# Performance work log

Hardware: AMD Instinct MI355X
Metric: run time of the kernel (lower is better)

## Reference

```python
import jax, jax.numpy as jnp
import numpy as np

B, N, HN, HE, H = 8, 128, 256, 128, 8
DH = HN // H
P = N * (N - 1) // 2


def _ln(x, g, b, eps=1e-5):
    m = jnp.mean(x, axis=-1, keepdims=True)
    v = jnp.mean((x - m) ** 2, axis=-1, keepdims=True)
    return (x - m) * jax.lax.rsqrt(v + eps) * g + b


def setup_inputs() -> dict:
    key = jax.random.key(0)
    ks = jax.random.split(key, 16)
    i1, i2 = np.triu_indices(N, k=1)  # all unordered pairs, P = N(N-1)/2
    s = lambda fan: 1.0 / np.sqrt(fan)
    return {
        "node_feat": jax.random.normal(ks[0], (B, N, HN), jnp.float32),
        "edge_feat": jax.random.normal(ks[1], (B, P, HE), jnp.float32),
        "x_idx1": jnp.asarray(i1, jnp.int32),
        "x_idx2": jnp.asarray(i2, jnp.int32),
        "mask_valid": jax.random.bernoulli(ks[2], 0.9, (B, P)).astype(jnp.float32),
        "Wqkv": jax.random.normal(ks[3], (HN, 3 * HN), jnp.float32) * s(HN),
        "bqkv": jnp.zeros((3 * HN,), jnp.float32),
        "Wev": jax.random.normal(ks[4], (HE, HN), jnp.float32) * s(HE),
        "bev": jnp.zeros((HN,), jnp.float32),
        "Wea": jax.random.normal(ks[5], (HE, H), jnp.float32) * s(HE),
        "bea": jnp.zeros((H,), jnp.float32),
        "Wo": jax.random.normal(ks[6], (2 * HN, HN), jnp.float32) * s(2 * HN),
        "bo": jnp.zeros((HN,), jnp.float32),
        "Wsk": jax.random.normal(ks[7], (HN, 2 * HN), jnp.float32) * s(HN),
        "bsk": jnp.zeros((2 * HN,), jnp.float32),
        "gn": jnp.ones((HN,), jnp.float32),
        "bn": jnp.zeros((HN,), jnp.float32),
        "ge": jnp.ones((HE,), jnp.float32),
        "be": jnp.zeros((HE,), jnp.float32),
    }


def reference(node_feat, edge_feat, x_idx1, x_idx2, mask_valid,
              Wqkv, bqkv, Wev, bev, Wea, bea, Wo, bo, Wsk, bsk,
              gn, bn, ge, be):
    n_in = _ln(node_feat, gn, bn)                      # [B,N,HN]
    e_in = _ln(edge_feat, ge, be)                      # [B,P,HE]
    q, k, v = jnp.split(n_in @ Wqkv + bqkv, 3, axis=-1)
    to_h = lambda t: t.reshape(B, -1, H, DH).transpose(0, 2, 1, 3)
    q, k, v = to_h(q), to_h(k), to_h(v)                # [B,H,N,DH]
    e_val = to_h(e_in @ Wev + bev)                     # [B,H,P,DH]
    e_adj = (e_in @ Wea + bea).transpose(0, 2, 1)      # [B,H,P]

    scale = DH ** -0.5
    logits = jnp.einsum('bhqd,bhkd->bhqk', q, k) * scale  # [B,H,N,N]
    # per-pair logits; torch stacks [qk, edge_adj] then sums -> just add
    l_node1 = logits[:, :, x_idx1, x_idx2] + e_adj     # node i1 attends to i2
    l_node2 = logits[:, :, x_idx2, x_idx1] + e_adj     # node i2 attends to i1
    v_node1 = e_val + v[:, :, x_idx2]                  # value node i1 receives
    v_node2 = e_val + v[:, :, x_idx1]

    # group the 2P directed edges by destination node (= torch cat+sort+reshape)
    cat_idx = jnp.concatenate([x_idx1, x_idx2])        # [2P]
    order = jnp.argsort(cat_idx)                       # stable sort
    gl = jnp.concatenate([l_node1, l_node2], axis=2)[:, :, order].reshape(B, H, N, N - 1)
    gv = jnp.concatenate([v_node1, v_node2], axis=2)[:, :, order].reshape(B, H, N, N - 1, DH)
    gm = jnp.concatenate([mask_valid, mask_valid], axis=1)[:, order].reshape(B, N, N - 1)[:, None]  # [B,1,N,N-1]

    gl = jnp.where(gm == 0.0, -9e15, gl)
    probs = jax.nn.softmax(gl, axis=3)
    probs = probs * jnp.any(gm != 0.0, axis=3, keepdims=True).astype(probs.dtype)
    attn = jnp.einsum('bhnk,bhnkd->bhnd', probs, gv)   # [B,H,N,DH]
    attn = attn.transpose(0, 2, 1, 3).reshape(B, N, HN)

    comb = jax.nn.gelu(jnp.concatenate([n_in, attn], axis=-1) @ Wo + bo, approximate=False)
    val, gate = jnp.split(comb @ Wsk + bsk, 2, axis=-1)
    g = jax.nn.sigmoid(gate)
    return node_feat * (1.0 - g) + val * g
```

## Files before the change

kernel.cpp:

```cpp
#include <hip/hip_runtime.h>
#include <hip/hip_bf16.h>
#include <math.h>

#define BB 8
#define NN 128
#define HN 256
#define HE 128
#define NH 8
#define DH 32
#define PP 8128
#define BP (BB*PP)

typedef __hip_bfloat16 bf16;
typedef __hip_bfloat162 bf162;
typedef __attribute__((ext_vector_type(8))) short bf16x8;
typedef __attribute__((ext_vector_type(4))) float f32x4;

__device__ __forceinline__ float bf2f(bf16 x){ return __bfloat162float(x); }
__device__ __forceinline__ float bfraw2f(short u){
  return __uint_as_float(((unsigned)(unsigned short)u) << 16);
}

__device__ __forceinline__ float wave_sum(float v){
  #pragma unroll
  for (int off=32; off>=1; off>>=1) v += __shfl_xor(v, off, 64);
  return v;
}
__device__ __forceinline__ float g16_sum(float v){
  #pragma unroll
  for (int off=8; off>=1; off>>=1) v += __shfl_xor(v, off, 16);
  return v;
}

__device__ __forceinline__ int pair_idx(int a, int c){
  int i = a < c ? a : c;
  int j = a < c ? c : a;
  return ((i*(255 - i))>>1) + (j - i - 1);
}

#define C_NODE 0LL
#define C_MASK 262144LL
#define C_WQKV 327168LL
#define C_BQKV 523776LL
#define C_WEV  524544LL
#define C_BEV  557312LL
#define C_WEA  557568LL
#define C_BEA  558592LL
#define C_WO   558600LL
#define C_BO   689672LL
#define C_WSK  689928LL
#define C_BSK  821000LL
#define C_GN   821512LL
#define C_BN   821768LL
#define C_GE   822024LL
#define C_BE   822152LL
#define IOFF   822400LL
#define TOT8   102785
#define CONVBLKS 402
#define I_NIN  0LL
#define I_Q    262144LL
#define I_K    524288LL
#define I_V    786432LL
#define I_ATTN 1048576LL
#define I_COMB 1310720LL
#define I_EA2  1572864LL
#define I_XG   2093056LL
#define I_WT   14577664LL
#define I_WOB  14594048LL
#define I_WSKB 14659584LL
#define I_FLG  14725120LL

struct SrcPtrs { const void* p[16]; };

__global__ __launch_bounds__(256) void k_convert(SrcPtrs sp, float* __restrict__ dst,
                                                 int* __restrict__ flags,
                                                 const unsigned short* __restrict__ nodeRaw,
                                                 const void* __restrict__ rawWev,
                                                 bf16* __restrict__ Wt,
                                                 const void* __restrict__ rawWo,
                                                 const void* __restrict__ rawWsk,
                                                 bf16* __restrict__ WoB,
                                                 bf16* __restrict__ WskB)
{
  __shared__ int sbad;
  if (threadIdx.x == 0) sbad = 0;
  __syncthreads();
  {
    int bad = 0;
    for (int i = threadIdx.x; i < 1024; i += 256){
      unsigned e = (nodeRaw[i] >> 7) & 0xFFu;
      if (e >= 194u) bad = 1;
    }
    if (bad) sbad = 1;
  }
  __syncthreads();
  const int f32 = sbad;
  if (blockIdx.x == 0 && threadIdx.x == 0) flags[0] = f32;

  if (blockIdx.x >= CONVBLKS + 128){
    int o = (blockIdx.x - (CONVBLKS + 128))*256 + threadIdx.x;
    const void* src = (o < 16384) ? rawWo : rawWsk;
    bf16* dw = (o < 16384) ? WoB : WskB;
    int lo = (o < 16384) ? o : o - 16384;
    if (f32){
      const float4* s4 = (const float4*)src;
      float4 a0 = s4[2*lo], a1 = s4[2*lo+1];
      union { float4 f; bf16 h[8]; } cv;
      cv.h[0]=__float2bfloat16(a0.x); cv.h[1]=__float2bfloat16(a0.y);
      cv.h[2]=__float2bfloat16(a0.z); cv.h[3]=__float2bfloat16(a0.w);
      cv.h[4]=__float2bfloat16(a1.x); cv.h[5]=__float2bfloat16(a1.y);
      cv.h[6]=__float2bfloat16(a1.z); cv.h[7]=__float2bfloat16(a1.w);
      *reinterpret_cast<float4*>(dw + lo*8) = cv.f;
    } else {
      *reinterpret_cast<float4*>(dw + lo*8) = ((const float4*)src)[lo];
    }
    return;
  }

  if (blockIdx.x >= CONVBLKS){
    int idx = (blockIdx.x - CONVBLKS)*256 + threadIdx.x;
    float v = f32 ? ((const float*)rawWev)[idx]
                  : bfraw2f(((const short*)rawWev)[idx]);
    Wt[(idx & 255)*128 + (idx >> 8)] = __float2bfloat16(v);
    return;
  }

  int o = blockIdx.x*256 + threadIdx.x;
  if (o >= TOT8) return;
  const int cum[17] = {0,32768,40896,65472,65568,69664,69696,69824,69825,
                       86209,86241,102625,102689,102721,102753,102769,102785};
  int s = 0;
  #pragma unroll
  for (int i = 1; i <= 15; i++) if (o >= cum[i]) s = i;
  const int li = o - cum[s];
  float4 r0, r1;
  if (f32){
    const float4* src = (const float4*)sp.p[s];
    r0 = src[2*li]; r1 = src[2*li+1];
  } else {
    union { float4 f; unsigned short u[8]; } cv;
    cv.f = ((const float4*)sp.p[s])[li];
    r0.x = __uint_as_float((unsigned)cv.u[0] << 16);
    r0.y = __uint_as_float((unsigned)cv.u[1] << 16);
    r0.z = __uint_as_float((unsigned)cv.u[2] << 16);
    r0.w = __uint_as_float((unsigned)cv.u[3] << 16);
    r1.x = __uint_as_float((unsigned)cv.u[4] << 16);
    r1.y = __uint_as_float((unsigned)cv.u[5] << 16);
    r1.z = __uint_as_float((unsigned)cv.u[6] << 16);
    r1.w = __uint_as_float((unsigned)cv.u[7] << 16);
  }
  float4* d = (float4*)(dst + (long long)cum[s]*8);
  d[2*li]   = r0;
  d[2*li+1] = r1;
}

__global__ __launch_bounds__(256) void k1_node_ln_qkv(
    const float* __restrict__ cnode, const float* __restrict__ cWqkv,
    const float* __restrict__ cbqkv, const float* __restrict__ cgn, const float* __restrict__ cbn,
    float* __restrict__ nin_ws, float* __restrict__ q_ws, float* __restrict__ k_ws,
    float* __restrict__ v_ws)
{
  __shared__ float xln[4][HN];
  const int t = threadIdx.x, wv = t>>6, lane = t&63;
  const int cb = blockIdx.x % 3;
  const int g0 = (blockIdx.x / 3) * 4;
  {
    int g = g0 + wv;
    float x[4];
    #pragma unroll
    for (int i=0;i<4;i++) x[i] = cnode[g*HN + lane + 64*i];
    float s = x[0]+x[1]+x[2]+x[3];
    s = wave_sum(s);
    float m = s * (1.0f/HN);
    float q = 0.f;
    #pragma unroll
    for (int i=0;i<4;i++){ float d = x[i]-m; q += d*d; }
    q = wave_sum(q);
    float rstd = rsqrtf(fmaxf(q*(1.0f/HN), 0.f) + 1e-5f);
    #pragma unroll
    for (int i=0;i<4;i++){
      int c = lane + 64*i;
      float y = (x[i]-m)*rstd*cgn[c] + cbn[c];
      xln[wv][c] = y;
      if (cb == 0) nin_ws[g*HN + c] = y;
    }
  }
  __syncthreads();
  const int col = cb*256 + t;
  float acc[4];
  {
    float bb = cbqkv[col];
    #pragma unroll
    for (int r=0;r<4;r++) acc[r] = bb;
  }
  for (int k=0;k<HN;k+=4){
    float4 xv[4];
    #pragma unroll
    for (int r=0;r<4;r++) xv[r] = *reinterpret_cast<const float4*>(&xln[r][k]);
    #pragma unroll
    for (int kk=0;kk<4;kk++){
      float w = cWqkv[(k+kk)*768 + col];
      #pragma unroll
      for (int r=0;r<4;r++) acc[r] = fmaf((&xv[r].x)[kk], w, acc[r]);
    }
  }
  if (cb == 2){
    #pragma unroll
    for (int r=0;r<4;r++) v_ws[(long)(g0+r)*HN + t] = acc[r];
  } else {
    float* dstp = (cb == 0) ? q_ws : k_ws;
    const int h = t>>5, d = t&31;
    #pragma unroll
    for (int r=0;r<4;r++){
      int g = g0 + r;
      int b = g>>7, n = g&127;
      dstp[((b*NH + h)*NN + n)*DH + d] = acc[r];
    }
  }
}

__global__ __launch_bounds__(256) void k2a_edge_ln(
    const void* __restrict__ edge_raw, const float* __restrict__ cWea,
    const float* __restrict__ cbea, const float* __restrict__ cge,
    const float* __restrict__ cbe, const float* __restrict__ cmask,
    bf16* __restrict__ xg, float* __restrict__ ea2, const int* __restrict__ flags)
{
  __shared__ float xlnS[16][136];
  __shared__ float part[128];
  const int t = threadIdx.x;
  const int R0 = blockIdx.x*16;
  const int b = R0 / PP;
  const int p0 = R0 - b*PP;
  const int f32 = flags[0];
  {
    int r = t>>4, sub = t&15;
    long base = (long)(R0 + r)*HE + sub*8;
    float x[8];
    if (f32){
      const float* cef = (const float*)edge_raw + base;
      float4 a0 = *reinterpret_cast<const float4*>(cef);
      float4 a1 = *reinterpret_cast<const float4*>(cef + 4);
      x[0]=a0.x; x[1]=a0.y; x[2]=a0.z; x[3]=a0.w;
      x[4]=a1.x; x[5]=a1.y; x[6]=a1.z; x[7]=a1.w;
    } else {
      union { float4 f; short u[8]; } cv;
      cv.f = *reinterpret_cast<const float4*>((const bf16*)edge_raw + base);
      #pragma unroll
      for (int i=0;i<8;i++) x[i] = bfraw2f(cv.u[i]);
    }
    float s = 0.f;
    #pragma unroll
    for (int i=0;i<8;i++) s += x[i];
    s = g16_sum(s);
    float m = s*(1.0f/HE);
    float q = 0.f;
    #pragma unroll
    for (int i=0;i<8;i++){ float dd = x[i]-m; q += dd*dd; }
    q = g16_sum(q);
    float rstd = rsqrtf(fmaxf(q*(1.0f/HE), 0.f) + 1e-5f);
    #pragma unroll
    for (int i=0;i<8;i++){
      int c = sub*8 + i;
      xlnS[r][c] = (x[i]-m)*rstd*cge[c] + cbe[c];
    }
  }
  __syncthreads();
  {
    int r = t>>4, c0 = (t&15)*8;
    union { float4 f; bf16 h[8]; } o;
    #pragma unroll
    for (int i=0;i<8;i++) o.h[i] = __float2bfloat16(xlnS[r][c0+i]);
    *reinterpret_cast<float4*>(xg + (long)(R0 + r)*HE + c0) = o.f;
  }
  {
    const int c = t & 7, r = (t>>3) & 15, half = t>>7;
    const int pid = r*8 + c;
    float s = half ? 0.0f : cbea[c];
    const int k0 = half*64;
    #pragma unroll 8
    for (int k=k0; k<k0+64; k++) s = fmaf(xlnS[r][k], cWea[k*NH + c], s);
    if (half){ part[pid] = s; }
    __syncthreads();
    if (!half){
      s += part[pid];
      int p = p0 + r;
      float mk = cmask[b*PP + p];
      ea2[((long)b*PP + p)*8 + c] = (mk != 0.0f) ? s : -9e15f;
    }
  }
}

__global__ __launch_bounds__(256) void k3_attn(
    const float* __restrict__ q_ws,
    const float* __restrict__ k_ws,
    const float* __restrict__ v_ws,
    const bf16* __restrict__ xg,
    const float* __restrict__ ea2,
    const bf16* __restrict__ Wt,
    const float* __restrict__ cbev,
    float* __restrict__ attn)
{
  __shared__ __align__(16) float qS[8][32];
  __shared__ __align__(16) int   prS[128];
  __shared__ __align__(16) float eaS[128][8];
  __shared__ __align__(16) float pS[8][128];
  __shared__ __align__(16) float sS[8][128];
  __shared__ __align__(16) bf16  xgS[128][128];
  __shared__ float anyS[8];
  const int t = threadIdx.x;
  const int bid = blockIdx.x;
  const int swz = (bid & 7)*128 + (bid >> 3);
  const int n = swz & 127, b = swz >> 7;
  const int h = t >> 5, ln = t & 31;

  qS[h][ln] = q_ws[(((long)b*NH + h)*NN + n)*DH + ln];
  if (t < 128){
    int m = t;
    prS[m] = pair_idx(n, (m == n) ? (m ^ 1) : m);
  }
  __syncthreads();

  const bf16* xgb = xg + (long)b*PP*HE;
  {
    int m = t >> 1, c0 = (t & 1)*4;
    float4 ev = *reinterpret_cast<const float4*>(ea2 + ((long)b*PP + prS[m])*8 + c0);
    *reinterpret_cast<float4*>(&eaS[m][c0]) = ev;
  }
  #pragma unroll
  for (int it=0; it<8; ++it){
    int idx = it*256 + t;
    int row = idx >> 4, seg = idx & 15;
    int pr = prS[row];
    *reinterpret_cast<float4*>(&xgS[row][seg*8]) =
        *reinterpret_cast<const float4*>(xgb + (long)pr*HE + seg*8);
  }
  __syncthreads();

  const float scale = 0.17677669529663687f;
  float4 qv[8];
  #pragma unroll
  for (int d4=0; d4<8; d4++) qv[d4] = *reinterpret_cast<const float4*>(&qS[h][d4*4]);
  const float* kb = k_ws + ((long)b*NH + h)*NN*DH;
  float l[4];
  float mx = -INFINITY;
  int valid = 0;
  #pragma unroll
  for (int j=0;j<4;j++){
    int m = ln + 32*j;
    const float* kr = kb + m*DH;
    float dot = 0.f;
    #pragma unroll
    for (int d4=0; d4<8; d4++){
      float4 kv = *reinterpret_cast<const float4*>(kr + d4*4);
      dot = fmaf((&qv[d4].x)[0], kv.x, dot);
      dot = fmaf((&qv[d4].x)[1], kv.y, dot);
      dot = fmaf((&qv[d4].x)[2], kv.z, dot);
      dot = fmaf((&qv[d4].x)[3], kv.w, dot);
    }
    float eav = eaS[m][h];
    bool self = (m == n);
    l[j] = self ? -INFINITY : fmaf(dot, scale, eav);
    if (!self && eav > -8.9e15f) valid = 1;
    mx = fmaxf(mx, l[j]);
  }
  #pragma unroll
  for (int off=16; off>=1; off>>=1) mx = fmaxf(mx, __shfl_xor(mx, off, 32));
  float e[4], s = 0.f;
  #pragma unroll
  for (int j=0;j<4;j++){ e[j] = __expf(l[j]-mx); s += e[j]; }
  float av = valid ? 1.f : 0.f;
  #pragma unroll
  for (int off=16; off>=1; off>>=1){
    s  += __shfl_xor(s,  off, 32);
    av += __shfl_xor(av, off, 32);
  }
  float inv = (av > 0.f) ? (1.0f/s) : 0.f;
  #pragma unroll
  for (int j=0;j<4;j++) pS[h][ln+32*j] = e[j]*inv;
  if (ln == 0) anyS[h] = (av > 0.f) ? 1.f : 0.f;
  __syncthreads();

  const float* vb = v_ws + (long)b*NN*HN + h*DH + ln;
  float S0=0.f,S1=0.f,S2=0.f,S3=0.f,T=0.f;
  #pragma unroll 2
  for (int m0=0; m0<128; m0+=4){
    float4 p4 = *reinterpret_cast<const float4*>(&pS[h][m0]);
    #pragma unroll
    for (int i=0;i<4;i++){
      float pm = (&p4.x)[i];
      short4 xv = *reinterpret_cast<const short4*>(&xgS[m0+i][ln*4]);
      S0 = fmaf(pm, bfraw2f(xv.x), S0);
      S1 = fmaf(pm, bfraw2f(xv.y), S1);
      S2 = fmaf(pm, bfraw2f(xv.z), S2);
      S3 = fmaf(pm, bfraw2f(xv.w), S3);
      T  = fmaf(pm, vb[(m0+i)*HN], T);
    }
  }
  {
    float4 sv; sv.x=S0; sv.y=S1; sv.z=S2; sv.w=S3;
    *reinterpret_cast<float4*>(&sS[h][ln*4]) = sv;
  }
  __syncthreads();

  float acc = T + anyS[h]*cbev[h*DH + ln];
  const bf16* wr = Wt + (h*DH + ln)*HE;
  #pragma unroll 4
  for (int k0=0;k0<128;k0+=8){
    float4 sa = *reinterpret_cast<const float4*>(&sS[h][k0]);
    float4 sb = *reinterpret_cast<const float4*>(&sS[h][k0+4]);
    bf16x8 wv = *reinterpret_cast<const bf16x8*>(wr + k0);
    acc = fmaf(sa.x, bfraw2f(wv[0]), acc);
    acc = fmaf(sa.y, bfraw2f(wv[1]), acc);
    acc = fmaf(sa.z, bfraw2f(wv[2]), acc);
    acc = fmaf(sa.w, bfraw2f(wv[3]), acc);
    acc = fmaf(sb.x, bfraw2f(wv[4]), acc);
    acc = fmaf(sb.y, bfraw2f(wv[5]), acc);
    acc = fmaf(sb.z, bfraw2f(wv[6]), acc);
    acc = fmaf(sb.w, bfraw2f(wv[7]), acc);
  }
  attn[((long)b*NN + n)*HN + h*DH + ln] = acc;
}

__global__ __launch_bounds__(256) void k4_wo_gelu(
    const float* __restrict__ nin_ws, const float* __restrict__ attn,
    const bf16* __restrict__ WoB, const float* __restrict__ cbo,
    float* __restrict__ comb)
{
  __shared__ float xc[4][512];
  __shared__ float ps[3][4][64];
  const int t = threadIdx.x;
  const int g0 = (blockIdx.x >> 2) * 4;
  const int cq = blockIdx.x & 3;
  {
    int r = t>>6, c0 = (t&63)*8;
    const float* src = (c0 < 256) ? (nin_ws + (long)(g0+r)*HN + c0)
                                  : (attn + (long)(g0+r)*HN + (c0-256));
    float4 a0 = *reinterpret_cast<const float4*>(src);
    float4 a1 = *reinterpret_cast<const float4*>(src+4);
    *reinterpret_cast<float4*>(&xc[r][c0]) = a0;
    *reinterpret_cast<float4*>(&xc[r][c0+4]) = a1;
  }
  __syncthreads();
  const int cidx = t & 63, ks = t >> 6;
  const int col = cq*64 + cidx;
  float acc[4] = {0.f,0.f,0.f,0.f};
  const int k0 = ks*128;
  #pragma unroll 4
  for (int k=k0; k<k0+128; k++){
    float w = bf2f(WoB[k*HN + col]);
    #pragma unroll
    for (int r=0;r<4;r++) acc[r] = fmaf(xc[r][k], w, acc[r]);
  }
  if (ks){
    #pragma unroll
    for (int r=0;r<4;r++) ps[ks-1][r][cidx] = acc[r];
  }
  __syncthreads();
  if (!ks){
    float bb = cbo[col];
    #pragma unroll
    for (int r=0;r<4;r++){
      float x = acc[r] + bb + ps[0][r][cidx] + ps[1][r][cidx] + ps[2][r][cidx];
      comb[(long)(g0+r)*HN + col] = 0.5f*x*(1.0f + erff(x*0.7071067811865475f));
    }
  }
}

__global__ __launch_bounds__(256) void k5_sk_gate(
    const float* __restrict__ comb, const float* __restrict__ cnode,
    const bf16* __restrict__ WskB, const float* __restrict__ cbsk,
    void* __restrict__ out, const int* __restrict__ flags)
{
  __shared__ float xc[4][HN];
  __shared__ float psv[3][4][64];
  __shared__ float psg[3][4][64];
  const int t = threadIdx.x;
  const int g0 = (blockIdx.x >> 2) * 4;
  const int cq = blockIdx.x & 3;
  {
    int r = t>>6, c0 = (t&63)*4;
    *reinterpret_cast<float4*>(&xc[r][c0]) =
        *reinterpret_cast<const float4*>(comb + (long)(g0+r)*HN + c0);
  }
  __syncthreads();
  const int cidx = t & 63, ks = t >> 6;
  const int col = cq*64 + cidx;
  float av[4] = {0.f,0.f,0.f,0.f}, ag[4] = {0.f,0.f,0.f,0.f};
  const int k0 = ks*64;
  #pragma unroll 4
  for (int k=k0; k<k0+64; k++){
    float wv = bf2f(WskB[k*512 + col]);
    float wg = bf2f(WskB[k*512 + col + 256]);
    #pragma unroll
    for (int r=0;r<4;r++){
      float xr = xc[r][k];
      av[r] = fmaf(xr, wv, av[r]);
      ag[r] = fmaf(xr, wg, ag[r]);
    }
  }
  if (ks){
    #pragma unroll
    for (int r=0;r<4;r++){ psv[ks-1][r][cidx] = av[r]; psg[ks-1][r][cidx] = ag[r]; }
  }
  __syncthreads();
  if (!ks){
    const int f32 = flags[0];
    float bv = cbsk[col], bg = cbsk[col+256];
    #pragma unroll
    for (int r=0;r<4;r++){
      float v = av[r] + bv + psv[0][r][cidx] + psv[1][r][cidx] + psv[2][r][cidx];
      float g = ag[r] + bg + psg[0][r][cidx] + psg[1][r][cidx] + psg[2][r][cidx];
      float gg = 1.0f/(1.0f + __expf(-g));
      float nf = cnode[(long)(g0+r)*HN + col];
      float res = nf*(1.0f - gg) + v*gg;
      if (f32) ((float*)out)[(long)(g0+r)*HN + col] = res;
      else ((bf16*)out)[(long)(g0+r)*HN + col] = __float2bfloat16(res);
    }
  }
}

extern "C" void kernel_launch(void* const* d_in, const int* in_sizes, int n_inputs,
                              void* d_out, int out_size, void* d_ws, size_t ws_size,
                              hipStream_t stream)
{
  float* ws = (float*)d_ws;
  float* c_node = ws + C_NODE;
  float* c_mask = ws + C_MASK;
  float* c_Wqkv = ws + C_WQKV;
  float* c_bqkv = ws + C_BQKV;
  float* c_bev  = ws + C_BEV;
  float* c_Wea  = ws + C_WEA;
  float* c_bea  = ws + C_BEA;
  float* c_bo   = ws + C_BO;
  float* c_bsk  = ws + C_BSK;
  float* c_gn   = ws + C_GN;
  float* c_bn   = ws + C_BN;
  float* c_ge   = ws + C_GE;
  float* c_be   = ws + C_BE;
  float* base   = ws + IOFF;
  float* nin_ws  = base + I_NIN;
  float* q_ws    = base + I_Q;
  float* k_ws    = base + I_K;
  float* v_ws    = base + I_V;
  float* attn_ws = base + I_ATTN;
  float* comb_ws = base + I_COMB;
  float* ea2_ws  = base + I_EA2;
  bf16*  xg_ws   = (bf16*)(base + I_XG);
  bf16*  wt_ws   = (bf16*)(base + I_WT);
  bf16*  wob_ws  = (bf16*)(base + I_WOB);
  bf16*  wskb_ws = (bf16*)(base + I_WSKB);
  int*   flags   = (int*)(base + I_FLG);

  SrcPtrs sp;
  sp.p[0]  = d_in[0];
  sp.p[1]  = d_in[4];
  sp.p[2]  = d_in[5];
  sp.p[3]  = d_in[6];
  sp.p[4]  = d_in[7];
  sp.p[5]  = d_in[8];
  sp.p[6]  = d_in[9];
  sp.p[7]  = d_in[10];
  sp.p[8]  = d_in[11];
  sp.p[9]  = d_in[12];
  sp.p[10] = d_in[13];
  sp.p[11] = d_in[14];
  sp.p[12] = d_in[15];
  sp.p[13] = d_in[16];
  sp.p[14] = d_in[17];
  sp.p[15] = d_in[18];

  k_convert<<<CONVBLKS + 256, 256, 0, stream>>>(sp, ws, flags,
                                                (const unsigned short*)d_in[0],
                                                d_in[7], wt_ws,
                                                d_in[11], d_in[13],
                                                wob_ws, wskb_ws);
  k1_node_ln_qkv<<<768, 256, 0, stream>>>(c_node, c_Wqkv, c_bqkv, c_gn, c_bn,
                                          nin_ws, q_ws, k_ws, v_ws);
  k2a_edge_ln<<<BP/16, 256, 0, stream>>>(d_in[1], c_Wea, c_bea, c_ge, c_be, c_mask,
                                         xg_ws, ea2_ws, flags);
  k3_attn<<<BB*NN, 256, 0, stream>>>(q_ws, k_ws, v_ws, xg_ws, ea2_ws, wt_ws, c_bev,
                                     attn_ws);
  k4_wo_gelu<<<1024, 256, 0, stream>>>(nin_ws, attn_ws, wob_ws, c_bo, comb_ws);
  k5_sk_gate<<<1024, 256, 0, stream>>>(comb_ws, c_node, wskb_ws, c_bsk, d_out, flags);
}
```

Before: 198.0 us.

## Prefetch gathered edge rows into registers and overlap with logit computation

The attention kernel now loads q and the edge logit bias straight from global memory into registers and removes the shared staging arrays for them, along with two block barriers. The gathered edge-feature rows are loaded into registers before the QK/softmax phase and written to shared memory only afterward, so global gather latency overlaps with the logit math. Softmax probabilities are broadcast with wave shuffles instead of shared memory, and an occupancy hint of 4 blocks is added. The cost is higher register pressure from holding 8 float4 prefetches plus q, which the launch-bounds hint may force into spills.

Measured after the change: 198.0 us. About the same (+0.0%).

```diff
diff --git a/kernel.cpp b/kernel.cpp
--- a/kernel.cpp
+++ b/kernel.cpp
@@ -290,7 +290,7 @@
   }
 }
 
-__global__ __launch_bounds__(256) void k3_attn(
+__global__ __launch_bounds__(256, 4) void k3_attn(
     const float* __restrict__ q_ws,
     const float* __restrict__ k_ws,
     const float* __restrict__ v_ws,
@@ -300,46 +300,38 @@
     const float* __restrict__ cbev,
     float* __restrict__ attn)
 {
-  __shared__ __align__(16) float qS[8][32];
-  __shared__ __align__(16) int   prS[128];
-  __shared__ __align__(16) float eaS[128][8];
-  __shared__ __align__(16) float pS[8][128];
+  __shared__ __align__(16) bf16  xgS[128][128];
   __shared__ __align__(16) float sS[8][128];
-  __shared__ __align__(16) bf16  xgS[128][128];
-  __shared__ float anyS[8];
   const int t = threadIdx.x;
   const int bid = blockIdx.x;
   const int swz = (bid & 7)*128 + (bid >> 3);
   const int n = swz & 127, b = swz >> 7;
   const int h = t >> 5, ln = t & 31;
 
-  qS[h][ln] = q_ws[(((long)b*NH + h)*NN + n)*DH + ln];
-  if (t < 128){
-    int m = t;
-    prS[m] = pair_idx(n, (m == n) ? (m ^ 1) : m);
-  }
-  __syncthreads();
-
+  float4 qv[8];
+  const float* qb = q_ws + (((long)b*NH + h)*NN + n)*DH;
+  #pragma unroll
+  for (int d4=0; d4<8; d4++) qv[d4] = *reinterpret_cast<const float4*>(qb + d4*4);
+  float eav[4];
+  const float* eab = ea2 + (long)b*PP*8;
+  #pragma unroll
+  for (int j=0;j<4;j++){
+    int m = ln + 32*j;
+    int ms = (m == n) ? (m ^ 1) : m;
+    eav[j] = eab[(long)pair_idx(n, ms)*8 + h];
+  }
   const bf16* xgb = xg + (long)b*PP*HE;
-  {
-    int m = t >> 1, c0 = (t & 1)*4;
-    float4 ev = *reinterpret_cast<const float4*>(ea2 + ((long)b*PP + prS[m])*8 + c0);
-    *reinterpret_cast<float4*>(&eaS[m][c0]) = ev;
-  }
+  const int rowb = t >> 4, seg = t & 15;
+  float4 xr[8];
   #pragma unroll
   for (int it=0; it<8; ++it){
-    int idx = it*256 + t;
-    int row = idx >> 4, seg = idx & 15;
-    int pr = prS[row];
-    *reinterpret_cast<float4*>(&xgS[row][seg*8]) =
-        *reinterpret_cast<const float4*>(xgb + (long)pr*HE + seg*8);
-  }
-  __syncthreads();
+    int row = it*16 + rowb;
+    int ms = (row == n) ? (row ^ 1) : row;
+    int pr = pair_idx(n, ms);
+    xr[it] = *reinterpret_cast<const float4*>(xgb + (long)pr*HE + seg*8);
+  }
 
   const float scale = 0.17677669529663687f;
-  float4 qv[8];
-  #pragma unroll
-  for (int d4=0; d4<8; d4++) qv[d4] = *reinterpret_cast<const float4*>(&qS[h][d4*4]);
   const float* kb = k_ws + ((long)b*NH + h)*NN*DH;
   float l[4];
   float mx = -INFINITY;
@@ -352,15 +344,14 @@
     #pragma unroll
     for (int d4=0; d4<8; d4++){
       float4 kv = *reinterpret_cast<const float4*>(kr + d4*4);
-      dot = fmaf((&qv[d4].x)[0], kv.x, dot);
-      dot = fmaf((&qv[d4].x)[1], kv.y, dot);
-      dot = fmaf((&qv[d4].x)[2], kv.z, dot);
-      dot = fmaf((&qv[d4].x)[3], kv.w, dot);
-    }
-    float eav = eaS[m][h];
+      dot = fmaf(qv[d4].x, kv.x, dot);
+      dot = fmaf(qv[d4].y, kv.y, dot);
+      dot = fmaf(qv[d4].z, kv.z, dot);
+      dot = fmaf(qv[d4].w, kv.w, dot);
+    }
     bool self = (m == n);
-    l[j] = self ? -INFINITY : fmaf(dot, scale, eav);
-    if (!self && eav > -8.9e15f) valid = 1;
+    l[j] = self ? -INFINITY : fmaf(dot, scale, eav[j]);
+    if (!self && eav[j] > -8.9e15f) valid = 1;
     mx = fmaxf(mx, l[j]);
   }
   #pragma unroll
@@ -375,25 +366,33 @@
     av += __shfl_xor(av, off, 32);
   }
   float inv = (av > 0.f) ? (1.0f/s) : 0.f;
-  #pragma unroll
-  for (int j=0;j<4;j++) pS[h][ln+32*j] = e[j]*inv;
-  if (ln == 0) anyS[h] = (av > 0.f) ? 1.f : 0.f;
+  float pj0 = e[0]*inv, pj1 = e[1]*inv, pj2 = e[2]*inv, pj3 = e[3]*inv;
+
+  #pragma unroll
+  for (int it=0; it<8; ++it){
+    int row = it*16 + rowb;
+    *reinterpret_cast<float4*>(&xgS[row][seg*8]) = xr[it];
+  }
   __syncthreads();
 
   const float* vb = v_ws + (long)b*NN*HN + h*DH + ln;
   float S0=0.f,S1=0.f,S2=0.f,S3=0.f,T=0.f;
-  #pragma unroll 2
-  for (int m0=0; m0<128; m0+=4){
-    float4 p4 = *reinterpret_cast<const float4*>(&pS[h][m0]);
-    #pragma unroll
-    for (int i=0;i<4;i++){
-      float pm = (&p4.x)[i];
-      short4 xv = *reinterpret_cast<const short4*>(&xgS[m0+i][ln*4]);
-      S0 = fmaf(pm, bfraw2f(xv.x), S0);
-      S1 = fmaf(pm, bfraw2f(xv.y), S1);
-      S2 = fmaf(pm, bfraw2f(xv.z), S2);
-      S3 = fmaf(pm, bfraw2f(xv.w), S3);
-      T  = fmaf(pm, vb[(m0+i)*HN], T);
+  #pragma unroll
+  for (int j=0;j<4;j++){
+    float pcur = (j==0) ? pj0 : (j==1) ? pj1 : (j==2) ? pj2 : pj3;
+    #pragma unroll 2
+    for (int mm=0; mm<32; mm+=4){
+      #pragma unroll
+      for (int i=0;i<4;i++){
+        int m = j*32 + mm + i;
+        float pm = __shfl(pcur, mm + i, 32);
+        short4 xv = *reinterpret_cast<const short4*>(&xgS[m][ln*4]);
+        S0 = fmaf(pm, bfraw2f(xv.x), S0);
+        S1 = fmaf(pm, bfraw2f(xv.y), S1);
+        S2 = fmaf(pm, bfraw2f(xv.z), S2);
+        S3 = fmaf(pm, bfraw2f(xv.w), S3);
+        T  = fmaf(pm, vb[m*HN], T);
+      }
     }
   }
   {
@@ -402,7 +401,7 @@
   }
   __syncthreads();
 
-  float acc = T + anyS[h]*cbev[h*DH + ln];
+  float acc = T + ((av > 0.f) ? cbev[h*DH + ln] : 0.f);
   const bf16* wr = Wt + (h*DH + ln)*HE;
   #pragma unroll 4
   for (int k0=0;k0<128;k0+=8){
```
